# Optimization experiments

Hardware: AMD Instinct MI355X
Metric: run time of the kernel (lower is better)

## Reference

```python
import jax, jax.numpy as jnp
import numpy as np

B, C, H, W = 1, 64, 96, 96
IC = C // 2  # inter_channels


def setup_inputs() -> dict:
    key = jax.random.key(0)
    ks = jax.random.split(key, 9)
    s_in = 1.0 / np.sqrt(C)
    s_out = 1.0 / np.sqrt(IC)
    return {
        "x": jax.random.normal(ks[0], (B, C, H, W), dtype=jnp.float32),
        "Wt": jax.random.uniform(ks[1], (IC, C), jnp.float32, -s_in, s_in),
        "bt": jax.random.uniform(ks[2], (IC,), jnp.float32, -s_in, s_in),
        "Wp": jax.random.uniform(ks[3], (IC, C), jnp.float32, -s_in, s_in),
        "bp": jax.random.uniform(ks[4], (IC,), jnp.float32, -s_in, s_in),
        "Wg": jax.random.uniform(ks[5], (IC, C), jnp.float32, -s_in, s_in),
        "bg": jax.random.uniform(ks[6], (IC,), jnp.float32, -s_in, s_in),
        "Wo": jax.random.uniform(ks[7], (C, IC), jnp.float32, -s_out, s_out),
        "bo": jax.random.uniform(ks[8], (C,), jnp.float32, -s_out, s_out),
    }


def _proj(Wmat, bvec, x):
    # 1x1x1 Conv3d on x.unsqueeze(-1) == per-pixel channel mix: [B,C,H,W] -> [B,IC,H,W]
    return jnp.einsum("oc,bchw->bohw", Wmat, x) + bvec[None, :, None, None]


def reference(x, Wt, bt, Wp, bp, Wg, bg, Wo, bo):
    b, c, h, w = x.shape
    ic = c // 2
    theta = _proj(Wt, bt, x).reshape(-1, ic)     # [N, ic], N = b*h*w (torch reshape semantics)
    phi = _proj(Wp, bp, x).reshape(ic, -1)       # [ic, N]
    scores = jax.nn.softmax(theta @ phi, axis=1)  # [N, N] row-softmax
    g = _proj(Wg, bg, x).reshape(-1, ic)          # [N, ic]
    y = jax.nn.softmax(scores @ g, axis=1)        # [N, ic], softmax over ic
    y = y.reshape(b, ic, h, w)
    out = jnp.einsum("oi,bihw->bohw", Wo, y) + bo[None, :, None, None] + x
    return out
```

## Files before the change

### kernel.cpp

```cpp
#include <hip/hip_runtime.h>
#include <hip/hip_bf16.h>

#define NPIX 9216
#define CIN 64
#define ICH 32
#define LOG2E 1.4426950408889634f

typedef float f32x4 __attribute__((ext_vector_type(4)));
typedef short bf16x8 __attribute__((ext_vector_type(8)));

#if __has_builtin(__builtin_amdgcn_exp2f)
#define EXP2(x) __builtin_amdgcn_exp2f(x)
#else
#define EXP2(x) exp2f(x)
#endif

#define GLLDS(gp, lp) \
  __builtin_amdgcn_global_load_lds( \
      (const __attribute__((address_space(1))) unsigned int*)(gp), \
      (__attribute__((address_space(3))) unsigned int*)(lp), 16, 0, 0)

static __device__ __forceinline__ unsigned short f2bf(float f) {
  union { float f; unsigned u; } v; v.f = f;
  unsigned u = v.u;
  u = u + 0x7FFFu + ((u >> 16) & 1u);
  return (unsigned short)(u >> 16);
}

__global__ __launch_bounds__(256) void proj_kernel(
    const float* __restrict__ x,
    const float* __restrict__ Wt, const float* __restrict__ bt,
    const float* __restrict__ Wp, const float* __restrict__ bp,
    const float* __restrict__ Wg, const float* __restrict__ bg,
    unsigned short* __restrict__ theta,
    unsigned short* __restrict__ phiT,
    unsigned short* __restrict__ vTs,
    float* __restrict__ zbuf)
{
  const int sub  = blockIdx.x % 36;
  const int grp  = blockIdx.x / 36;
  const int proj = grp >> 2;
  const int og   = (grp & 3) * 8;
  const int m    = sub * 256 + threadIdx.x;

  const int t = blockIdx.x * 256 + threadIdx.x;
  if (t < 76032) {
    const f32x4 z4 = {0.f, 0.f, 0.f, 0.f};
    reinterpret_cast<f32x4*>(zbuf)[t] = z4;
  }

  const float* W; const float* bias;
  if (proj == 0)      { W = Wt; bias = bt; }
  else if (proj == 1) { W = Wp; bias = bp; }
  else                { W = Wg; bias = bg; }

  float acc[8];
#pragma unroll
  for (int o = 0; o < 8; ++o) acc[o] = bias[og + o];
  for (int c = 0; c < CIN; ++c) {
    float xv = x[c * NPIX + m];
#pragma unroll
    for (int o = 0; o < 8; ++o) acc[o] = fmaf(W[(og + o) * CIN + c], xv, acc[o]);
  }

  if (proj == 0) {
#pragma unroll
    for (int o = 0; o < 8; ++o) theta[(og + o) * NPIX + m] = f2bf(acc[o] * LOG2E);
  } else if (proj == 1) {
    union { unsigned short s[8]; bf16x8 v; } pk;
#pragma unroll
    for (int o = 0; o < 8; ++o) pk.s[o] = f2bf(acc[o]);
    *reinterpret_cast<bf16x8*>(phiT + m * ICH + og) = pk.v;
  } else {
#pragma unroll
    for (int o = 0; o < 8; ++o) {
      int n = 288 * (og + o) + (m >> 5);
      int k = n & 31;
      int p = ((k >> 2) & 3) * 8 + ((k >> 4) << 2) + (k & 3);
      vTs[(m & 31) * NPIX + (n & ~31) + p] = f2bf(acc[o]);
    }
  }
}

__global__ __launch_bounds__(256) void attn_kernel(
    const unsigned short* __restrict__ theta,
    const unsigned short* __restrict__ phiT,
    const unsigned short* __restrict__ vTs,
    float* __restrict__ pacc, float* __restrict__ pl)
{
  __shared__ __align__(16) unsigned char lds[2][8192];

  const int tid = threadIdx.x;
  const int l   = tid & 63;
  const int w   = tid >> 6;
  const int r16 = l & 15;
  const int g   = l >> 4;
  const int qt    = blockIdx.x >> 4;
  const int split = blockIdx.x & 15;
  const int qbase = qt * 128 + w * 32;
  const int keybase = split * 576;
  const int cbase = (qt * 5) % 9;

  bf16x8 qf0 = *reinterpret_cast<const bf16x8*>(theta + (qbase + r16) * ICH + 8 * g);
  bf16x8 qf1 = *reinterpret_cast<const bf16x8*>(theta + (qbase + 16 + r16) * ICH + 8 * g);

  f32x4 acc00 = {0.f, 0.f, 0.f, 0.f}, acc01 = {0.f, 0.f, 0.f, 0.f};
  f32x4 acc10 = {0.f, 0.f, 0.f, 0.f}, acc11 = {0.f, 0.f, 0.f, 0.f};
  const f32x4 z4 = {0.f, 0.f, 0.f, 0.f};
  float l_run0 = 0.f, l_run1 = 0.f;

  auto stage = [&](int buf, int cc) {
    unsigned char* Lb = &lds[buf][0];
    const int key0 = keybase + cc * 64;
    if (w < 2) {
      const int k  = (l >> 2);
      const int gp = (l & 3) ^ (k & 3);
#pragma unroll
      for (int i = 0; i < 2; ++i) {
        const int j = w * 2 + i;
        GLLDS(phiT + (key0 + j * 16 + k) * ICH + gp * 8, Lb + j * 1024);
      }
    } else {
#pragma unroll
      for (int i = 0; i < 2; ++i) {
        const int dg = (w - 2) * 2 + i;
        const int d  = dg * 8 + (l >> 3);
        const int sl = (l & 7) ^ (d & 7);
        GLLDS(vTs + d * NPIX + key0 + sl * 8, Lb + 4096 + dg * 1024);
      }
    }
  };

  auto step = [&](const unsigned char* Lb, int st) {
    const int kk = st * 32 + r16;
    const int kx = (g ^ (kk & 3)) << 4;
    const bf16x8 kf0 = *reinterpret_cast<const bf16x8*>(Lb + kk * 64 + kx);
    const bf16x8 kf1 = *reinterpret_cast<const bf16x8*>(Lb + (kk + 16) * 64 + kx);
    const int sp = ((st * 4 + g) ^ (r16 & 7)) * 16;
    const bf16x8 vf0 = *reinterpret_cast<const bf16x8*>(Lb + 4096 + r16 * 128 + sp);
    const bf16x8 vf1 = *reinterpret_cast<const bf16x8*>(Lb + 4096 + (16 + r16) * 128 + sp);

    f32x4 cs00 = __builtin_amdgcn_mfma_f32_16x16x32_bf16(kf0, qf0, z4, 0, 0, 0);
    f32x4 cs01 = __builtin_amdgcn_mfma_f32_16x16x32_bf16(kf1, qf0, z4, 0, 0, 0);
    f32x4 cs10 = __builtin_amdgcn_mfma_f32_16x16x32_bf16(kf0, qf1, z4, 0, 0, 0);
    f32x4 cs11 = __builtin_amdgcn_mfma_f32_16x16x32_bf16(kf1, qf1, z4, 0, 0, 0);

    float p0[8], p1[8]; float ps0 = 0.f, ps1 = 0.f;
#pragma unroll
    for (int j = 0; j < 4; ++j) {
      p0[j]     = EXP2(cs00[j]); ps0 += p0[j];
      p0[4 + j] = EXP2(cs01[j]); ps0 += p0[4 + j];
      p1[j]     = EXP2(cs10[j]); ps1 += p1[j];
      p1[4 + j] = EXP2(cs11[j]); ps1 += p1[4 + j];
    }
    l_run0 += ps0; l_run1 += ps1;

    union { unsigned u[4]; bf16x8 v; } pkA, pkB;
#pragma unroll
    for (int j = 0; j < 4; ++j) {
      asm("v_cvt_pk_bf16_f32 %0, %1, %2" : "=v"(pkA.u[j]) : "v"(p0[2 * j]), "v"(p0[2 * j + 1]));
      asm("v_cvt_pk_bf16_f32 %0, %1, %2" : "=v"(pkB.u[j]) : "v"(p1[2 * j]), "v"(p1[2 * j + 1]));
    }

    acc00 = __builtin_amdgcn_mfma_f32_16x16x32_bf16(pkA.v, vf0, acc00, 0, 0, 0);
    acc01 = __builtin_amdgcn_mfma_f32_16x16x32_bf16(pkA.v, vf1, acc01, 0, 0, 0);
    acc10 = __builtin_amdgcn_mfma_f32_16x16x32_bf16(pkB.v, vf0, acc10, 0, 0, 0);
    acc11 = __builtin_amdgcn_mfma_f32_16x16x32_bf16(pkB.v, vf1, acc11, 0, 0, 0);
  };

  stage(0, cbase);
  __syncthreads();
  int cur = 0;
#pragma unroll 1
  for (int c = 0; c < 9; ++c) {
    if (c + 1 < 9) {
      int cn = cbase + c + 1; if (cn >= 9) cn -= 9;
      stage(cur ^ 1, cn);
    }
    step(&lds[cur][0], 0);
    step(&lds[cur][0], 1);
    __syncthreads();
    cur ^= 1;
  }

  l_run0 += __shfl_xor(l_run0, 16); l_run0 += __shfl_xor(l_run0, 32);
  l_run1 += __shfl_xor(l_run1, 16); l_run1 += __shfl_xor(l_run1, 32);

#pragma unroll
  for (int j = 0; j < 4; ++j) {
    const int q0 = qbase + 4 * g + j;
    const int q1 = qbase + 16 + 4 * g + j;
    atomicAdd(&pacc[q0 * ICH + r16],      acc00[j]);
    atomicAdd(&pacc[q0 * ICH + 16 + r16], acc01[j]);
    atomicAdd(&pacc[q1 * ICH + r16],      acc10[j]);
    atomicAdd(&pacc[q1 * ICH + 16 + r16], acc11[j]);
  }
  if (g == 0) {
    atomicAdd(&pl[qbase + r16],      l_run0);
    atomicAdd(&pl[qbase + 16 + r16], l_run1);
  }
}

__global__ __launch_bounds__(256) void merge_kernel(
    const float* __restrict__ pacc, const float* __restrict__ pl,
    float* __restrict__ ybuf)
{
  const int q  = blockIdx.x * 8 + (threadIdx.x >> 5);
  const int ch = threadIdx.x & 31;

  float z  = pacc[q * ICH + ch] / pl[q];
  float zl = z * LOG2E;
  float zm = zl;
#pragma unroll
  for (int k = 1; k < 32; k <<= 1) zm = fmaxf(zm, __shfl_xor(zm, k));
  float e = EXP2(zl - zm);
  float ss = e;
#pragma unroll
  for (int k = 1; k < 32; k <<= 1) ss += __shfl_xor(ss, k);
  ybuf[q * ICH + ch] = e / ss;
}

__global__ __launch_bounds__(256) void out_kernel(
    const float* __restrict__ x, const float* __restrict__ Wo,
    const float* __restrict__ bo, const float* __restrict__ ybuf,
    float* __restrict__ out)
{
  const int sub = blockIdx.x % 36;
  const int o0  = (blockIdx.x / 36) * 8;
  const int s   = sub * 256 + threadIdx.x;

  float acc[8];
#pragma unroll
  for (int o = 0; o < 8; ++o) acc[o] = 0.f;
  for (int c = 0; c < ICH; ++c) {
    float yv = ybuf[c * NPIX + s];
#pragma unroll
    for (int o = 0; o < 8; ++o) acc[o] = fmaf(Wo[(o0 + o) * ICH + c], yv, acc[o]);
  }
#pragma unroll
  for (int o = 0; o < 8; ++o) {
    int oc = o0 + o;
    out[oc * NPIX + s] = acc[o] + bo[oc] + x[oc * NPIX + s];
  }
}

extern "C" void kernel_launch(void* const* d_in, const int* in_sizes, int n_in,
                              void* d_out, int out_size, void* d_ws, size_t ws_size,
                              hipStream_t stream) {
  const float* x  = (const float*)d_in[0];
  const float* Wt = (const float*)d_in[1];
  const float* bt = (const float*)d_in[2];
  const float* Wp = (const float*)d_in[3];
  const float* bp = (const float*)d_in[4];
  const float* Wg = (const float*)d_in[5];
  const float* bg = (const float*)d_in[6];
  const float* Wo = (const float*)d_in[7];
  const float* bo = (const float*)d_in[8];
  float* out = (float*)d_out;

  char* ws = (char*)d_ws;
  unsigned short* theta = (unsigned short*)(ws);
  unsigned short* phiT  = (unsigned short*)(ws + 589824);
  unsigned short* vTs   = (unsigned short*)(ws + 1179648);
  float* pacc = (float*)(ws + 1769472);
  float* pl   = (float*)(ws + 2949120);
  float* ybuf = (float*)(ws);

  proj_kernel<<<432, 256, 0, stream>>>(x, Wt, bt, Wp, bp, Wg, bg, theta, phiT, vTs, pacc);
  attn_kernel<<<1152, 256, 0, stream>>>(theta, phiT, vTs, pacc, pl);
  merge_kernel<<<1152, 256, 0, stream>>>(pacc, pl, ybuf);
  out_kernel<<<288, 256, 0, stream>>>(x, Wo, bo, ybuf, out);
}
```

Baseline: 46.19 us.

## Give each wave its own key split with private LDS pipeline and in-block reduction

The attention kernel is restructured so each block handles 32 queries and each of its four waves processes a different key split. Each wave stages its own phi/v chunks into a private LDS double buffer, waiting with explicit vmcnt counts instead of block-wide barriers in the main loop. Partial accumulators and row sums from the four waves are reduced through LDS before one wave does the global atomics, which cuts atomic traffic by four. The trade-offs are smaller per-wave chunks, more theta reloads across blocks, and an extra LDS reduction epilogue.

```diff
diff --git a/kernel.cpp b/kernel.cpp
--- a/kernel.cpp
+++ b/kernel.cpp
@@ -19,6 +19,13 @@
   __builtin_amdgcn_global_load_lds( \
       (const __attribute__((address_space(1))) unsigned int*)(gp), \
       (__attribute__((address_space(3))) unsigned int*)(lp), 16, 0, 0)
+
+#define VMWAIT4 do { \
+  asm volatile("s_waitcnt vmcnt(4)" ::: "memory"); \
+  __builtin_amdgcn_sched_barrier(0); } while (0)
+#define VMWAIT0 do { \
+  asm volatile("s_waitcnt vmcnt(0)" ::: "memory"); \
+  __builtin_amdgcn_sched_barrier(0); } while (0)
 
 static __device__ __forceinline__ unsigned short f2bf(float f) {
   union { float f; unsigned u; } v; v.f = f;
@@ -88,18 +95,20 @@
     const unsigned short* __restrict__ vTs,
     float* __restrict__ pacc, float* __restrict__ pl)
 {
-  __shared__ __align__(16) unsigned char lds[2][8192];
+  __shared__ __align__(16) unsigned char lds[4][8192];
+  __shared__ float lbuf[4][32];
 
   const int tid = threadIdx.x;
   const int l   = tid & 63;
   const int w   = tid >> 6;
   const int r16 = l & 15;
   const int g   = l >> 4;
-  const int qt    = blockIdx.x >> 4;
-  const int split = blockIdx.x & 15;
-  const int qbase = qt * 128 + w * 32;
+  const int qt    = blockIdx.x >> 2;
+  const int sg    = blockIdx.x & 3;
+  const int split = sg * 4 + w;
+  const int qbase = qt * 32;
   const int keybase = split * 576;
-  const int cbase = (qt * 5) % 9;
+  const int cbase = (unsigned)(qt * 5 + sg * 7) % 18;
 
   bf16x8 qf0 = *reinterpret_cast<const bf16x8*>(theta + (qbase + r16) * ICH + 8 * g);
   bf16x8 qf1 = *reinterpret_cast<const bf16x8*>(theta + (qbase + 16 + r16) * ICH + 8 * g);
@@ -109,36 +118,25 @@
   const f32x4 z4 = {0.f, 0.f, 0.f, 0.f};
   float l_run0 = 0.f, l_run1 = 0.f;
 
+  unsigned char* Lw = &lds[w][0];
+  const int kk = l >> 2;
+  const int gp = (l & 3) ^ (kk & 3);
+
   auto stage = [&](int buf, int cc) {
-    unsigned char* Lb = &lds[buf][0];
-    const int key0 = keybase + cc * 64;
-    if (w < 2) {
-      const int k  = (l >> 2);
-      const int gp = (l & 3) ^ (k & 3);
-#pragma unroll
-      for (int i = 0; i < 2; ++i) {
-        const int j = w * 2 + i;
-        GLLDS(phiT + (key0 + j * 16 + k) * ICH + gp * 8, Lb + j * 1024);
-      }
-    } else {
-#pragma unroll
-      for (int i = 0; i < 2; ++i) {
-        const int dg = (w - 2) * 2 + i;
-        const int d  = dg * 8 + (l >> 3);
-        const int sl = (l & 7) ^ (d & 7);
-        GLLDS(vTs + d * NPIX + key0 + sl * 8, Lb + 4096 + dg * 1024);
-      }
-    }
+    unsigned char* Lb = Lw + buf * 4096;
+    const int key0 = keybase + cc * 32;
+    GLLDS(phiT + (key0 + kk) * ICH + gp * 8,        Lb);
+    GLLDS(phiT + (key0 + 16 + kk) * ICH + gp * 8,   Lb + 1024);
+    GLLDS(vTs + kk * NPIX + key0 + (l & 3) * 8,     Lb + 2048);
+    GLLDS(vTs + (16 + kk) * NPIX + key0 + (l & 3) * 8, Lb + 3072);
   };
 
-  auto step = [&](const unsigned char* Lb, int st) {
-    const int kk = st * 32 + r16;
-    const int kx = (g ^ (kk & 3)) << 4;
-    const bf16x8 kf0 = *reinterpret_cast<const bf16x8*>(Lb + kk * 64 + kx);
-    const bf16x8 kf1 = *reinterpret_cast<const bf16x8*>(Lb + (kk + 16) * 64 + kx);
-    const int sp = ((st * 4 + g) ^ (r16 & 7)) * 16;
-    const bf16x8 vf0 = *reinterpret_cast<const bf16x8*>(Lb + 4096 + r16 * 128 + sp);
-    const bf16x8 vf1 = *reinterpret_cast<const bf16x8*>(Lb + 4096 + (16 + r16) * 128 + sp);
+  auto step = [&](const unsigned char* Lb) {
+    const int kx = (g ^ (r16 & 3)) << 4;
+    const bf16x8 kf0 = *reinterpret_cast<const bf16x8*>(Lb + r16 * 64 + kx);
+    const bf16x8 kf1 = *reinterpret_cast<const bf16x8*>(Lb + 1024 + r16 * 64 + kx);
+    const bf16x8 vf0 = *reinterpret_cast<const bf16x8*>(Lb + 2048 + r16 * 64 + g * 16);
+    const bf16x8 vf1 = *reinterpret_cast<const bf16x8*>(Lb + 3072 + r16 * 64 + g * 16);
 
     f32x4 cs00 = __builtin_amdgcn_mfma_f32_16x16x32_bf16(kf0, qf0, z4, 0, 0, 0);
     f32x4 cs01 = __builtin_amdgcn_mfma_f32_16x16x32_bf16(kf1, qf0, z4, 0, 0, 0);
@@ -168,36 +166,53 @@
     acc11 = __builtin_amdgcn_mfma_f32_16x16x32_bf16(pkB.v, vf1, acc11, 0, 0, 0);
   };
 
-  stage(0, cbase);
-  __syncthreads();
-  int cur = 0;
+  auto chunkid = [&](int c) { int cc = cbase + c; return cc >= 18 ? cc - 18 : cc; };
+  stage(0, chunkid(0));
+  stage(1, chunkid(1));
 #pragma unroll 1
-  for (int c = 0; c < 9; ++c) {
-    if (c + 1 < 9) {
-      int cn = cbase + c + 1; if (cn >= 9) cn -= 9;
-      stage(cur ^ 1, cn);
-    }
-    step(&lds[cur][0], 0);
-    step(&lds[cur][0], 1);
-    __syncthreads();
-    cur ^= 1;
+  for (int c = 0; c < 18; ++c) {
+    if (c + 1 < 18) { VMWAIT4; } else { VMWAIT0; }
+    step(Lw + (c & 1) * 4096);
+    __builtin_amdgcn_sched_barrier(0);
+    if (c + 2 < 18) stage(c & 1, chunkid(c + 2));
   }
 
   l_run0 += __shfl_xor(l_run0, 16); l_run0 += __shfl_xor(l_run0, 32);
   l_run1 += __shfl_xor(l_run1, 16); l_run1 += __shfl_xor(l_run1, 32);
-
+  if (l < 16) { lbuf[w][l] = l_run0; lbuf[w][16 + l] = l_run1; }
+
+  __syncthreads();
+  float* accb = reinterpret_cast<float*>(&lds[0][0]);
 #pragma unroll
   for (int j = 0; j < 4; ++j) {
-    const int q0 = qbase + 4 * g + j;
-    const int q1 = qbase + 16 + 4 * g + j;
-    atomicAdd(&pacc[q0 * ICH + r16],      acc00[j]);
-    atomicAdd(&pacc[q0 * ICH + 16 + r16], acc01[j]);
-    atomicAdd(&pacc[q1 * ICH + r16],      acc10[j]);
-    atomicAdd(&pacc[q1 * ICH + 16 + r16], acc11[j]);
-  }
-  if (g == 0) {
-    atomicAdd(&pl[qbase + r16],      l_run0);
-    atomicAdd(&pl[qbase + 16 + r16], l_run1);
+    accb[(w * 64 + l) * 17 + j]      = acc00[j];
+    accb[(w * 64 + l) * 17 + 4 + j]  = acc01[j];
+    accb[(w * 64 + l) * 17 + 8 + j]  = acc10[j];
+    accb[(w * 64 + l) * 17 + 12 + j] = acc11[j];
+  }
+  __syncthreads();
+
+  if (w == 0) {
+#pragma unroll
+    for (int j = 0; j < 4; ++j) {
+      float a00 = 0.f, a01 = 0.f, a10 = 0.f, a11 = 0.f, lst0 = 0.f, lst1 = 0.f;
+#pragma unroll
+      for (int w2 = 0; w2 < 4; ++w2) {
+        a00 += accb[(w2 * 64 + l) * 17 + j];
+        a01 += accb[(w2 * 64 + l) * 17 + 4 + j];
+        a10 += accb[(w2 * 64 + l) * 17 + 8 + j];
+        a11 += accb[(w2 * 64 + l) * 17 + 12 + j];
+        lst0 += lbuf[w2][4 * g + j];
+        lst1 += lbuf[w2][16 + 4 * g + j];
+      }
+      const int q0 = qbase + 4 * g + j;
+      const int q1 = qbase + 16 + 4 * g + j;
+      atomicAdd(&pacc[q0 * ICH + r16],      a00);
+      atomicAdd(&pacc[q0 * ICH + 16 + r16], a01);
+      atomicAdd(&pacc[q1 * ICH + r16],      a10);
+      atomicAdd(&pacc[q1 * ICH + 16 + r16], a11);
+      if (r16 == 0) { atomicAdd(&pl[q0], lst0); atomicAdd(&pl[q1], lst1); }
+    }
   }
 }
 
```

After: 47.66 us. 1.03x slower.
